# Kernel tuning notes

Hardware: AMD Instinct MI355X
Metric: run time of the kernel (lower is better)

## Reference

```python
import jax, jax.numpy as jnp
import numpy as np

B, F, V, D = 4096, 26, 10000, 64
NUMB = 13
D0 = F * D            # 1664, cross/embedding width
IN = D0 + NUMB        # 1677, deep stack input width
HID = [1024, 512, 256]
EPS = 1e-5


def _bn(x, p):
    # eval-mode BatchNorm1d: p rows = [gamma, beta, running_mean, running_var]
    g, b, m, v = p[0], p[1], p[2], p[3]
    return (x - m) / jnp.sqrt(v + EPS) * g + b


def setup_inputs() -> dict:
    key = jax.random.key(0)
    ks = jax.random.split(key, 18)
    lin = lambda k, o, i: jax.random.normal(k, (o, i), jnp.float32) / np.sqrt(i).astype(np.float32)
    bn = lambda k, d: jax.random.uniform(k, (4, d), jnp.float32)
    return {
        "numb_features": jax.random.normal(ks[0], (B, NUMB), jnp.float32),
        "cat_features": jax.random.randint(ks[1], (B, F), 0, V),
        "emb_tables": jax.random.normal(ks[2], (F, V, D), jnp.float32) * 0.1,
        "bn0": bn(ks[3], IN),
        "w1": lin(ks[4], HID[0], IN), "b1": jax.random.normal(ks[5], (HID[0],)) * 0.01,
        "bn1": bn(ks[6], HID[0]),
        "w2": lin(ks[7], HID[1], HID[0]), "b2": jax.random.normal(ks[8], (HID[1],)) * 0.01,
        "bn2": bn(ks[9], HID[1]),
        "w3": lin(ks[10], HID[2], HID[1]), "b3": jax.random.normal(ks[11], (HID[2],)) * 0.01,
        "bn3": bn(ks[12], HID[2]),
        "cross_w": jax.random.normal(ks[13], (3, D0), jnp.float32) / np.sqrt(D0).astype(np.float32),
        "cross_b": jax.random.normal(ks[14], (3,), jnp.float32) * 0.01,
        "pred_w": lin(ks[15], 1, HID[2] + D0),
        "pred_b": jax.random.normal(ks[16], (1,), jnp.float32) * 0.01,
    }


def reference(numb_features, cat_features, emb_tables, bn0, w1, b1, bn1,
              w2, b2, bn2, w3, b3, bn3, cross_w, cross_b, pred_w, pred_b):
    # embedding lookup: [B, F, D] -> x0 [B, F*D]
    emb = emb_tables[jnp.arange(F)[None, :], cat_features]
    x0 = emb.reshape(B, D0)

    # cross layers: bmm(emb^T, emb) @ w + b + emb == emb*(emb.w) + b + emb (rank-1 form)
    x = x0
    for i in range(3):
        x = x * (x @ cross_w[i])[:, None] + cross_b[i] + x

    # deep stack: BN -> (Linear -> BN -> Dropout[eval=id]) x3
    h = jnp.concatenate([x0, numb_features], axis=1)
    h = _bn(h, bn0)
    h = _bn(h @ w1.T + b1, bn1)
    h = _bn(h @ w2.T + b2, bn2)
    h = _bn(h @ w3.T + b3, bn3)

    out = jnp.concatenate([x, h], axis=1) @ pred_w.T + pred_b
    return jax.nn.sigmoid(out)
```

## Files before the change

kernel.cpp:

```cpp
#include <hip/hip_runtime.h>
#include <math.h>

#define BATCH 4096
#define NFEAT 26
#define VOCAB 10000
#define EDIM 64
#define D0 1664
#define NUMB 13
#define IN_DIM 1677
#define H1D 1024
#define H2D 512
#define H3D 256
#define EPS 1e-5f



__global__ __launch_bounds__(256) void collapseA(
    const float* __restrict__ w3, const float* __restrict__ b3,
    const float* __restrict__ bn3, const float* __restrict__ pw,
    const float* __restrict__ b2, const float* __restrict__ bn2,
    const float* __restrict__ cw,
    float* __restrict__ u2, float* __restrict__ CvA,
    float* __restrict__ C3s, float* __restrict__ Csums,
    float* __restrict__ zero_region) {
    const int bid = blockIdx.x, tid = threadIdx.x;
    __shared__ float a3s[H3D];
    __shared__ float part[256];
    __shared__ float red[4][4];

    for (int i = tid; i < 2817; i += 256) zero_region[i] = 0.f;

    if (bid < 16) {
        {
            const int c = tid;
            float s3 = bn3[c] * rsqrtf(bn3[3 * H3D + c] + EPS);
            a3s[c] = pw[D0 + c] * s3;
        }
        __syncthreads();
        const int kk = tid & 31, seg = tid >> 5;
        const int k = bid * 32 + kk;
        float acc = 0.f;
#pragma unroll
        for (int i = 0; i < 32; ++i) {
            int c = seg * 32 + i;
            acc += a3s[c] * w3[(size_t)c * H2D + k];
        }
        part[tid] = acc;
        __syncthreads();
        if (tid < 32) {
            float s = 0.f;
#pragma unroll
            for (int sg = 0; sg < 8; ++sg) s += part[sg * 32 + tid];
            const int kq = bid * 32 + tid;
            u2[kq] = s;
            float s2 = bn2[kq] * rsqrtf(bn2[3 * H2D + kq] + EPS);
            float beta2 = (b2[kq] - bn2[2 * H2D + kq]) * s2 + bn2[H2D + kq];
            float pc = s * beta2;
            for (int o = 16; o > 0; o >>= 1) pc += __shfl_down(pc, o, 32);
            if (tid == 0) CvA[bid] = pc;
        }
    } else {
        float p0 = 0.f, p1 = 0.f, p2 = 0.f, p3 = 0.f;
        for (int j = tid; j < D0; j += 256) {
            p0 += cw[j]; p1 += cw[D0 + j]; p2 += cw[2 * D0 + j]; p3 += pw[j];
        }
        for (int o = 32; o > 0; o >>= 1) {
            p0 += __shfl_down(p0, o, 64); p1 += __shfl_down(p1, o, 64);
            p2 += __shfl_down(p2, o, 64); p3 += __shfl_down(p3, o, 64);
        }
        if ((tid & 63) == 0) {
            int w = tid >> 6;
            red[w][0] = p0; red[w][1] = p1; red[w][2] = p2; red[w][3] = p3;
        }
        __syncthreads();
        if (tid < 4) Csums[tid] = red[0][tid] + red[1][tid] + red[2][tid] + red[3][tid];
        __syncthreads();
        float c3;
        {
            const int c = tid;
            float s3 = bn3[c] * rsqrtf(bn3[3 * H3D + c] + EPS);
            c3 = pw[D0 + c] * ((b3[c] - bn3[2 * H3D + c]) * s3 + bn3[H3D + c]);
        }
        for (int o = 32; o > 0; o >>= 1) c3 += __shfl_down(c3, o, 64);
        if ((tid & 63) == 0) red[tid >> 6][0] = c3;
        __syncthreads();
        if (tid == 0) C3s[0] = red[0][0] + red[1][0] + red[2][0] + red[3][0];
    }
}

__global__ __launch_bounds__(256) void collapseB(
    const float* __restrict__ w2, const float* __restrict__ bn2,
    const float* __restrict__ u2,
    const float* __restrict__ b1, const float* __restrict__ bn1,
    const float* __restrict__ CvA, const float* __restrict__ C3s,
    float* __restrict__ u1, float* __restrict__ Cv) {
    const int bid = blockIdx.x, tid = threadIdx.x;
    __shared__ float a2s[32];
    __shared__ float red[4];
    const int p0 = (bid >> 2) * 32;
    if (tid < 32) {
        const int p = p0 + tid;
        float s2 = bn2[p] * rsqrtf(bn2[3 * H2D + p] + EPS);
        a2s[tid] = u2[p] * s2;
    }
    __syncthreads();
    const int n = (bid & 3) * 256 + tid;
    float acc = 0.f;
#pragma unroll
    for (int p = 0; p < 32; ++p)
        acc += a2s[p] * w2[(size_t)(p0 + p) * H1D + n];
    atomicAdd(&u1[n], acc);
    float s1 = bn1[n] * rsqrtf(bn1[3 * H1D + n] + EPS);
    float beta1 = (b1[n] - bn1[2 * H1D + n]) * s1 + bn1[H1D + n];
    float pc = acc * beta1;
    for (int o = 32; o > 0; o >>= 1) pc += __shfl_down(pc, o, 64);
    if ((tid & 63) == 0) red[tid >> 6] = pc;
    __syncthreads();
    if (tid == 0) atomicAdd(Cv, red[0] + red[1] + red[2] + red[3]);
    if (bid == 0 && tid < 16) {
        float v = CvA[tid];
        for (int o = 8; o > 0; o >>= 1) v += __shfl_down(v, o, 16);
        if (tid == 0) atomicAdd(Cv, v + C3s[0]);
    }
}

__global__ __launch_bounds__(256) void collapseC(
    const float* __restrict__ w1, const float* __restrict__ bn1,
    const float* __restrict__ u1, const float* __restrict__ bn0,
    float* __restrict__ u0, float* __restrict__ Cv) {
    const int bid = blockIdx.x, tid = threadIdx.x;
    __shared__ float a1s[64];
    __shared__ float red[4];
    const int jc = bid % 7, n0 = (bid / 7) * 64;
    if (tid < 64) {
        const int n = n0 + tid;
        float s1 = bn1[n] * rsqrtf(bn1[3 * H1D + n] + EPS);
        a1s[tid] = u1[n] * s1;
    }
    __syncthreads();
    const int j = jc * 256 + tid;
    float pc = 0.f;
    if (j < IN_DIM) {
        float acc = 0.f;
#pragma unroll 8
        for (int n = 0; n < 64; ++n)
            acc += a1s[n] * w1[(size_t)(n0 + n) * IN_DIM + j];
        atomicAdd(&u0[j], acc);
        float s0 = bn0[j] * rsqrtf(bn0[3 * IN_DIM + j] + EPS);
        float t0 = bn0[IN_DIM + j] - bn0[2 * IN_DIM + j] * s0;
        pc = acc * t0;
    }
    for (int o = 32; o > 0; o >>= 1) pc += __shfl_down(pc, o, 64);
    if ((tid & 63) == 0) red[tid >> 6] = pc;
    __syncthreads();
    if (tid == 0) atomicAdd(Cv, red[0] + red[1] + red[2] + red[3]);
}

__global__ __launch_bounds__(256) void fuse_out(
    const float* __restrict__ numb, const int* __restrict__ cat,
    const float* __restrict__ emb, const float* __restrict__ bn0,
    const float* __restrict__ cw, const float* __restrict__ cb,
    const float* __restrict__ pw, const float* __restrict__ pb,
    const float* __restrict__ u0, const float* __restrict__ Cv,
    const float* __restrict__ Csums, float* __restrict__ out) {
    __shared__ __align__(16) float vj[IN_DIM + 3];
    __shared__ int idx[8][NFEAT];
    const int bid = blockIdx.x, tid = threadIdx.x;
    const int b0 = bid * 8;

    for (int j = tid; j < IN_DIM; j += 256) {
        float s0 = bn0[j] * rsqrtf(bn0[3 * IN_DIM + j] + EPS);
        vj[j] = u0[j] * s0;
    }
    if (tid < 8 * NFEAT)
        idx[tid / NFEAT][tid % NFEAT] = cat[(b0 + tid / NFEAT) * NFEAT + tid % NFEAT];
    __syncthreads();

    const int wave = tid >> 6, lane = tid & 63;
    const float4* cw0 = (const float4*)cw;
    const float4* cw1 = (const float4*)(cw + D0);
    const float4* cw2 = (const float4*)(cw + 2 * D0);
    const float4* pw4 = (const float4*)pw;

#pragma unroll
    for (int rr = 0; rr < 2; rr++) {
        const int r = wave * 2 + rr, b = b0 + r;
        float d0 = 0.f, d1 = 0.f, d2 = 0.f, dp = 0.f, dv = 0.f;
        for (int j = lane; j < D0 / 4; j += 64) {
            int f = j >> 4, d4 = j & 15;
            float4 v = *(const float4*)&emb[((size_t)f * VOCAB + idx[r][f]) * EDIM + d4 * 4];
            float4 c0 = cw0[j], c1 = cw1[j], c2 = cw2[j], p4 = pw4[j];
            float4 vv = *(const float4*)&vj[j * 4];
            d0 += v.x * c0.x + v.y * c0.y + v.z * c0.z + v.w * c0.w;
            d1 += v.x * c1.x + v.y * c1.y + v.z * c1.z + v.w * c1.w;
            d2 += v.x * c2.x + v.y * c2.y + v.z * c2.z + v.w * c2.w;
            dp += v.x * p4.x + v.y * p4.y + v.z * p4.z + v.w * p4.w;
            dv += v.x * vv.x + v.y * vv.y + v.z * vv.z + v.w * vv.w;
        }
        for (int o = 32; o > 0; o >>= 1) {
            d0 += __shfl_down(d0, o, 64); d1 += __shfl_down(d1, o, 64);
            d2 += __shfl_down(d2, o, 64); dp += __shfl_down(dp, o, 64);
            dv += __shfl_down(dv, o, 64);
        }
        if (lane == 0) {
            float dn = 0.f;
#pragma unroll
            for (int t = 0; t < NUMB; ++t) dn += numb[b * NUMB + t] * vj[D0 + t];
            float P = 1.f, Q = 0.f;
            float dd[3] = {d0, d1, d2};
#pragma unroll
            for (int i = 0; i < 3; i++) {
                float s = 1.f + P * dd[i] + Q * Csums[i];
                P = s * P;
                Q = s * Q + cb[i];
            }
            float z = P * dp + Q * Csums[3] + dv + dn + Cv[0] + pb[0];
            out[b] = 1.f / (1.f + expf(-z));
        }
    }
}

extern "C" void kernel_launch(void* const* d_in, const int* in_sizes, int n_in,
                              void* d_out, int out_size, void* d_ws, size_t ws_size,
                              hipStream_t stream) {
    const float* numb = (const float*)d_in[0];
    const int* cat = (const int*)d_in[1];
    const float* emb = (const float*)d_in[2];
    const float* bn0 = (const float*)d_in[3];
    const float* w1 = (const float*)d_in[4];
    const float* b1 = (const float*)d_in[5];
    const float* bn1 = (const float*)d_in[6];
    const float* w2 = (const float*)d_in[7];
    const float* b2 = (const float*)d_in[8];
    const float* bn2 = (const float*)d_in[9];
    const float* w3 = (const float*)d_in[10];
    const float* b3 = (const float*)d_in[11];
    const float* bn3 = (const float*)d_in[12];
    const float* cw = (const float*)d_in[13];
    const float* cb = (const float*)d_in[14];
    const float* pw = (const float*)d_in[15];
    const float* pb = (const float*)d_in[16];
    float* out = (float*)d_out;

    char* ws = (char*)d_ws;
    float* u2    = (float*)(ws + 0);
    float* u1    = (float*)(ws + 2048);
    float* u0    = (float*)(ws + 6144);
    float* Cv    = (float*)(ws + 13312);
    float* CvA   = (float*)(ws + 13376);
    float* C3s   = (float*)(ws + 13440);
    float* Csums = (float*)(ws + 13456);
    float* zero_region = u1;

    collapseA<<<17, 256, 0, stream>>>(w3, b3, bn3, pw, b2, bn2, cw,
                                      u2, CvA, C3s, Csums, zero_region);
    collapseB<<<64, 256, 0, stream>>>(w2, bn2, u2, b1, bn1, CvA, C3s, u1, Cv);
    collapseC<<<112, 256, 0, stream>>>(w1, bn1, u1, bn0, u0, Cv);
    fuse_out<<<512, 256, 0, stream>>>(numb, cat, emb, bn0, cw, cb, pw, pb,
                                      u0, Cv, Csums, out);
}
```

Baseline: 150.0 us.

## Fuse four collapse/output kernels into one persistent kernel with flag-based inter-block sync

```diff
diff --git a/kernel.cpp b/kernel.cpp
--- a/kernel.cpp
+++ b/kernel.cpp
@@ -14,166 +14,177 @@
 #define EPS 1e-5f
 
 
-
-__global__ __launch_bounds__(256) void collapseA(
-    const float* __restrict__ w3, const float* __restrict__ b3,
-    const float* __restrict__ bn3, const float* __restrict__ pw,
-    const float* __restrict__ b2, const float* __restrict__ bn2,
-    const float* __restrict__ cw,
-    float* __restrict__ u2, float* __restrict__ CvA,
-    float* __restrict__ C3s, float* __restrict__ Csums,
-    float* __restrict__ zero_region) {
-    const int bid = blockIdx.x, tid = threadIdx.x;
-    __shared__ float a3s[H3D];
-    __shared__ float part[256];
-    __shared__ float red[4][4];
-
-    for (int i = tid; i < 2817; i += 256) zero_region[i] = 0.f;
-
-    if (bid < 16) {
-        {
-            const int c = tid;
-            float s3 = bn3[c] * rsqrtf(bn3[3 * H3D + c] + EPS);
-            a3s[c] = pw[D0 + c] * s3;
-        }
-        __syncthreads();
-        const int kk = tid & 31, seg = tid >> 5;
-        const int k = bid * 32 + kk;
-        float acc = 0.f;
-#pragma unroll
-        for (int i = 0; i < 32; ++i) {
-            int c = seg * 32 + i;
-            acc += a3s[c] * w3[(size_t)c * H2D + k];
-        }
-        part[tid] = acc;
-        __syncthreads();
-        if (tid < 32) {
-            float s = 0.f;
-#pragma unroll
-            for (int sg = 0; sg < 8; ++sg) s += part[sg * 32 + tid];
-            const int kq = bid * 32 + tid;
-            u2[kq] = s;
-            float s2 = bn2[kq] * rsqrtf(bn2[3 * H2D + kq] + EPS);
-            float beta2 = (b2[kq] - bn2[2 * H2D + kq]) * s2 + bn2[H2D + kq];
-            float pc = s * beta2;
-            for (int o = 16; o > 0; o >>= 1) pc += __shfl_down(pc, o, 32);
-            if (tid == 0) CvA[bid] = pc;
-        }
-    } else {
-        float p0 = 0.f, p1 = 0.f, p2 = 0.f, p3 = 0.f;
-        for (int j = tid; j < D0; j += 256) {
-            p0 += cw[j]; p1 += cw[D0 + j]; p2 += cw[2 * D0 + j]; p3 += pw[j];
-        }
-        for (int o = 32; o > 0; o >>= 1) {
-            p0 += __shfl_down(p0, o, 64); p1 += __shfl_down(p1, o, 64);
-            p2 += __shfl_down(p2, o, 64); p3 += __shfl_down(p3, o, 64);
-        }
-        if ((tid & 63) == 0) {
-            int w = tid >> 6;
-            red[w][0] = p0; red[w][1] = p1; red[w][2] = p2; red[w][3] = p3;
-        }
-        __syncthreads();
-        if (tid < 4) Csums[tid] = red[0][tid] + red[1][tid] + red[2][tid] + red[3][tid];
-        __syncthreads();
-        float c3;
-        {
-            const int c = tid;
-            float s3 = bn3[c] * rsqrtf(bn3[3 * H3D + c] + EPS);
-            c3 = pw[D0 + c] * ((b3[c] - bn3[2 * H3D + c]) * s3 + bn3[H3D + c]);
-        }
-        for (int o = 32; o > 0; o >>= 1) c3 += __shfl_down(c3, o, 64);
-        if ((tid & 63) == 0) red[tid >> 6][0] = c3;
-        __syncthreads();
-        if (tid == 0) C3s[0] = red[0][0] + red[1][0] + red[2][0] + red[3][0];
-    }
-}
-
-__global__ __launch_bounds__(256) void collapseB(
-    const float* __restrict__ w2, const float* __restrict__ bn2,
-    const float* __restrict__ u2,
-    const float* __restrict__ b1, const float* __restrict__ bn1,
-    const float* __restrict__ CvA, const float* __restrict__ C3s,
-    float* __restrict__ u1, float* __restrict__ Cv) {
-    const int bid = blockIdx.x, tid = threadIdx.x;
-    __shared__ float a2s[32];
-    __shared__ float red[4];
-    const int p0 = (bid >> 2) * 32;
-    if (tid < 32) {
-        const int p = p0 + tid;
-        float s2 = bn2[p] * rsqrtf(bn2[3 * H2D + p] + EPS);
-        a2s[tid] = u2[p] * s2;
+#define NC 113
+#define NFUSE 512
+#define GRID_BLKS (NC + NFUSE)
+#define TA 16
+#define TB 64
+#define TC 113
+
+__device__ __forceinline__ void wait_flag(int* f, int target) {
+    if (threadIdx.x == 0) {
+        while (__hip_atomic_load(f, __ATOMIC_ACQUIRE, __HIP_MEMORY_SCOPE_AGENT) < target)
+            __builtin_amdgcn_s_sleep(4);
+        __threadfence();
     }
     __syncthreads();
-    const int n = (bid & 3) * 256 + tid;
-    float acc = 0.f;
-#pragma unroll
-    for (int p = 0; p < 32; ++p)
-        acc += a2s[p] * w2[(size_t)(p0 + p) * H1D + n];
-    atomicAdd(&u1[n], acc);
-    float s1 = bn1[n] * rsqrtf(bn1[3 * H1D + n] + EPS);
-    float beta1 = (b1[n] - bn1[2 * H1D + n]) * s1 + bn1[H1D + n];
-    float pc = acc * beta1;
-    for (int o = 32; o > 0; o >>= 1) pc += __shfl_down(pc, o, 64);
-    if ((tid & 63) == 0) red[tid >> 6] = pc;
+}
+
+__device__ __forceinline__ void post_flag(int* f) {
     __syncthreads();
-    if (tid == 0) atomicAdd(Cv, red[0] + red[1] + red[2] + red[3]);
-    if (bid == 0 && tid < 16) {
-        float v = CvA[tid];
-        for (int o = 8; o > 0; o >>= 1) v += __shfl_down(v, o, 16);
-        if (tid == 0) atomicAdd(Cv, v + C3s[0]);
-    }
-}
-
-__global__ __launch_bounds__(256) void collapseC(
-    const float* __restrict__ w1, const float* __restrict__ bn1,
-    const float* __restrict__ u1, const float* __restrict__ bn0,
-    float* __restrict__ u0, float* __restrict__ Cv) {
-    const int bid = blockIdx.x, tid = threadIdx.x;
-    __shared__ float a1s[64];
-    __shared__ float red[4];
-    const int jc = bid % 7, n0 = (bid / 7) * 64;
-    if (tid < 64) {
-        const int n = n0 + tid;
-        float s1 = bn1[n] * rsqrtf(bn1[3 * H1D + n] + EPS);
-        a1s[tid] = u1[n] * s1;
-    }
-    __syncthreads();
-    const int j = jc * 256 + tid;
-    float pc = 0.f;
-    if (j < IN_DIM) {
-        float acc = 0.f;
-#pragma unroll 8
-        for (int n = 0; n < 64; ++n)
-            acc += a1s[n] * w1[(size_t)(n0 + n) * IN_DIM + j];
-        atomicAdd(&u0[j], acc);
-        float s0 = bn0[j] * rsqrtf(bn0[3 * IN_DIM + j] + EPS);
-        float t0 = bn0[IN_DIM + j] - bn0[2 * IN_DIM + j] * s0;
-        pc = acc * t0;
-    }
-    for (int o = 32; o > 0; o >>= 1) pc += __shfl_down(pc, o, 64);
-    if ((tid & 63) == 0) red[tid >> 6] = pc;
-    __syncthreads();
-    if (tid == 0) atomicAdd(Cv, red[0] + red[1] + red[2] + red[3]);
-}
-
-__global__ __launch_bounds__(256) void fuse_out(
+    if (threadIdx.x == 0) {
+        __threadfence();
+        __hip_atomic_fetch_add(f, 1, __ATOMIC_RELEASE, __HIP_MEMORY_SCOPE_AGENT);
+    }
+}
+
+__global__ __launch_bounds__(256, 4) void mega(
     const float* __restrict__ numb, const int* __restrict__ cat,
     const float* __restrict__ emb, const float* __restrict__ bn0,
+    const float* __restrict__ w1, const float* __restrict__ b1,
+    const float* __restrict__ bn1,
+    const float* __restrict__ w2, const float* __restrict__ b2,
+    const float* __restrict__ bn2,
+    const float* __restrict__ w3, const float* __restrict__ b3,
+    const float* __restrict__ bn3,
     const float* __restrict__ cw, const float* __restrict__ cb,
     const float* __restrict__ pw, const float* __restrict__ pb,
-    const float* __restrict__ u0, const float* __restrict__ Cv,
-    const float* __restrict__ Csums, float* __restrict__ out) {
-    __shared__ __align__(16) float vj[IN_DIM + 3];
-    __shared__ int idx[8][NFEAT];
+    float* __restrict__ u2, float* __restrict__ u1, float* __restrict__ u0,
+    float* __restrict__ Cv, int* __restrict__ flags,
+    float* __restrict__ Csums, float* __restrict__ out) {
     const int bid = blockIdx.x, tid = threadIdx.x;
-    const int b0 = bid * 8;
+    int* fA = flags + 0;
+    int* fB = flags + 1;
+    int* fC = flags + 2;
+
+    __shared__ __align__(16) float sA[1792];
+    __shared__ float sRed[4][4];
+    __shared__ int sIdx[8][NFEAT];
+
+    if (bid < NC) {
+        if (bid == 112) {
+            float p0 = 0.f, p1 = 0.f, p2 = 0.f, p3 = 0.f;
+            for (int j = tid; j < D0; j += 256) {
+                p0 += cw[j]; p1 += cw[D0 + j]; p2 += cw[2 * D0 + j]; p3 += pw[j];
+            }
+            for (int o = 32; o > 0; o >>= 1) {
+                p0 += __shfl_down(p0, o, 64); p1 += __shfl_down(p1, o, 64);
+                p2 += __shfl_down(p2, o, 64); p3 += __shfl_down(p3, o, 64);
+            }
+            if ((tid & 63) == 0) {
+                int w = tid >> 6;
+                sRed[w][0] = p0; sRed[w][1] = p1; sRed[w][2] = p2; sRed[w][3] = p3;
+            }
+            __syncthreads();
+            if (tid < 4) Csums[tid] = sRed[0][tid] + sRed[1][tid] + sRed[2][tid] + sRed[3][tid];
+            __syncthreads();
+            float c3;
+            {
+                const int c = tid;
+                float s3 = bn3[c] * rsqrtf(bn3[3 * H3D + c] + EPS);
+                c3 = pw[D0 + c] * ((b3[c] - bn3[2 * H3D + c]) * s3 + bn3[H3D + c]);
+            }
+            for (int o = 32; o > 0; o >>= 1) c3 += __shfl_down(c3, o, 64);
+            if ((tid & 63) == 0) sRed[tid >> 6][0] = c3;
+            __syncthreads();
+            if (tid == 0) atomicAdd(Cv, sRed[0][0] + sRed[1][0] + sRed[2][0] + sRed[3][0]);
+            post_flag(fC);
+            return;
+        }
+
+        if (bid < 16) {
+            {
+                float s3 = bn3[tid] * rsqrtf(bn3[3 * H3D + tid] + EPS);
+                sA[tid] = pw[D0 + tid] * s3;
+            }
+            __syncthreads();
+            const int kk = tid & 31, seg = tid >> 5;
+            const int k = bid * 32 + kk;
+            float acc = 0.f;
+#pragma unroll
+            for (int i = 0; i < 32; ++i) {
+                int c = seg * 32 + i;
+                acc += sA[c] * w3[(size_t)c * H2D + k];
+            }
+            sA[256 + tid] = acc;
+            __syncthreads();
+            if (tid < 32) {
+                float s = 0.f;
+#pragma unroll
+                for (int sg = 0; sg < 8; ++sg) s += sA[256 + sg * 32 + tid];
+                const int kq = bid * 32 + tid;
+                u2[kq] = s;
+                float s2 = bn2[kq] * rsqrtf(bn2[3 * H2D + kq] + EPS);
+                float beta2 = (b2[kq] - bn2[2 * H2D + kq]) * s2 + bn2[H2D + kq];
+                float pc = s * beta2;
+                for (int o = 16; o > 0; o >>= 1) pc += __shfl_down(pc, o, 32);
+                if (tid == 0) atomicAdd(Cv, pc);
+            }
+            post_flag(fA);
+        }
+
+        if (bid < 64) {
+            wait_flag(fA, TA);
+            const int p0 = (bid >> 2) * 32;
+            if (tid < 32) {
+                const int p = p0 + tid;
+                float s2 = bn2[p] * rsqrtf(bn2[3 * H2D + p] + EPS);
+                sA[1024 + tid] = u2[p] * s2;
+            }
+            __syncthreads();
+            const int n = (bid & 3) * 256 + tid;
+            float acc = 0.f;
+#pragma unroll
+            for (int p = 0; p < 32; ++p)
+                acc += sA[1024 + p] * w2[(size_t)(p0 + p) * H1D + n];
+            atomicAdd(&u1[n], acc);
+            float s1 = bn1[n] * rsqrtf(bn1[3 * H1D + n] + EPS);
+            float beta1 = (b1[n] - bn1[2 * H1D + n]) * s1 + bn1[H1D + n];
+            float pc = acc * beta1;
+            for (int o = 32; o > 0; o >>= 1) pc += __shfl_down(pc, o, 64);
+            if ((tid & 63) == 0) sRed[tid >> 6][0] = pc;
+            __syncthreads();
+            if (tid == 0) atomicAdd(Cv, sRed[0][0] + sRed[1][0] + sRed[2][0] + sRed[3][0]);
+            post_flag(fB);
+        }
+
+        wait_flag(fB, TB);
+        const int jc = bid % 7, n0c = (bid / 7) * 64;
+        if (tid < 64) {
+            const int n = n0c + tid;
+            float s1 = bn1[n] * rsqrtf(bn1[3 * H1D + n] + EPS);
+            sA[tid] = u1[n] * s1;
+        }
+        __syncthreads();
+        const int j = jc * 256 + tid;
+        float pc = 0.f;
+        if (j < IN_DIM) {
+            float acc = 0.f;
+#pragma unroll 8
+            for (int n = 0; n < 64; ++n)
+                acc += sA[n] * w1[(size_t)(n0c + n) * IN_DIM + j];
+            atomicAdd(&u0[j], acc);
+            float s0 = bn0[j] * rsqrtf(bn0[3 * IN_DIM + j] + EPS);
+            float t0 = bn0[IN_DIM + j] - bn0[2 * IN_DIM + j] * s0;
+            pc = acc * t0;
+        }
+        for (int o = 32; o > 0; o >>= 1) pc += __shfl_down(pc, o, 64);
+        if ((tid & 63) == 0) sRed[tid >> 6][0] = pc;
+        __syncthreads();
+        if (tid == 0) atomicAdd(Cv, sRed[0][0] + sRed[1][0] + sRed[2][0] + sRed[3][0]);
+        post_flag(fC);
+        return;
+    }
+
+    const int b0 = (bid - NC) * 8;
+    if (tid < 8 * NFEAT)
+        sIdx[tid / NFEAT][tid % NFEAT] = cat[(b0 + tid / NFEAT) * NFEAT + tid % NFEAT];
+    wait_flag(fC, TC);
 
     for (int j = tid; j < IN_DIM; j += 256) {
         float s0 = bn0[j] * rsqrtf(bn0[3 * IN_DIM + j] + EPS);
-        vj[j] = u0[j] * s0;
-    }
-    if (tid < 8 * NFEAT)
-        idx[tid / NFEAT][tid % NFEAT] = cat[(b0 + tid / NFEAT) * NFEAT + tid % NFEAT];
+        sA[j] = u0[j] * s0;
+    }
     __syncthreads();
 
     const int wave = tid >> 6, lane = tid & 63;
@@ -188,9 +199,9 @@
         float d0 = 0.f, d1 = 0.f, d2 = 0.f, dp = 0.f, dv = 0.f;
         for (int j = lane; j < D0 / 4; j += 64) {
             int f = j >> 4, d4 = j & 15;
-            float4 v = *(const float4*)&emb[((size_t)f * VOCAB + idx[r][f]) * EDIM + d4 * 4];
+            float4 v = *(const float4*)&emb[((size_t)f * VOCAB + sIdx[r][f]) * EDIM + d4 * 4];
             float4 c0 = cw0[j], c1 = cw1[j], c2 = cw2[j], p4 = pw4[j];
-            float4 vv = *(const float4*)&vj[j * 4];
+            float4 vv = *(const float4*)&sA[j * 4];
             d0 += v.x * c0.x + v.y * c0.y + v.z * c0.z + v.w * c0.w;
             d1 += v.x * c1.x + v.y * c1.y + v.z * c1.z + v.w * c1.w;
             d2 += v.x * c2.x + v.y * c2.y + v.z * c2.z + v.w * c2.w;
@@ -205,7 +216,7 @@
         if (lane == 0) {
             float dn = 0.f;
 #pragma unroll
-            for (int t = 0; t < NUMB; ++t) dn += numb[b * NUMB + t] * vj[D0 + t];
+            for (int t = 0; t < NUMB; ++t) dn += numb[b * NUMB + t] * sA[D0 + t];
             float P = 1.f, Q = 0.f;
             float dd[3] = {d0, d1, d2};
 #pragma unroll
@@ -247,15 +258,11 @@
     float* u1    = (float*)(ws + 2048);
     float* u0    = (float*)(ws + 6144);
     float* Cv    = (float*)(ws + 13312);
-    float* CvA   = (float*)(ws + 13376);
-    float* C3s   = (float*)(ws + 13440);
-    float* Csums = (float*)(ws + 13456);
-    float* zero_region = u1;
-
-    collapseA<<<17, 256, 0, stream>>>(w3, b3, bn3, pw, b2, bn2, cw,
-                                      u2, CvA, C3s, Csums, zero_region);
-    collapseB<<<64, 256, 0, stream>>>(w2, bn2, u2, b1, bn1, CvA, C3s, u1, Cv);
-    collapseC<<<112, 256, 0, stream>>>(w1, bn1, u1, bn0, u0, Cv);
-    fuse_out<<<512, 256, 0, stream>>>(numb, cat, emb, bn0, cw, cb, pw, pb,
-                                      u0, Cv, Csums, out);
-}
+    int*   flags = (int*)(ws + 13328);
+    float* Csums = (float*)(ws + 13344);
+
+    hipMemsetAsync(ws + 2048, 0, 11296, stream);
+    mega<<<GRID_BLKS, 256, 0, stream>>>(
+        numb, cat, emb, bn0, w1, b1, bn1, w2, b2, bn2, w3, b3, bn3,
+        cw, cb, pw, pb, u2, u1, u0, Cv, flags, Csums, out);
+}
```

New measurement: 297.6 us. +98.4%, slower.
